# Performance work log

Hardware: AMD Instinct MI355X
Metric: run time of the kernel (lower is better)

## Reference

```python
import jax, jax.numpy as jnp
import numpy as np

N_NODES = 100000


def _graph_conv_right(feat, src, dst, W, b, n_nodes):
    # DGL GraphConv(norm='right'): since in_feats > out_feats, apply weight first,
    # then sum-aggregate messages over edges, divide by in-degree (clamped >= 1),
    # add bias, then relu activation.
    h = feat @ W                                   # [N, out]
    msg = jnp.take(h, src, axis=0)                 # [E, out] gather from source nodes
    agg = jax.ops.segment_sum(msg, dst, num_segments=n_nodes)  # [N, out]
    deg = jax.ops.segment_sum(jnp.ones_like(dst, dtype=feat.dtype), dst,
                              num_segments=n_nodes)
    deg = jnp.clip(deg, 1.0, None)                 # allow_zero_in_degree
    out = agg / deg[:, None] + b
    return jax.nn.relu(out)


def setup_inputs() -> dict:
    key = jax.random.key(0)
    ks = jax.random.split(key, 6)
    n_edges = 3200000
    in_dim, hidden_dim, out_dim = 128, 32, 12
    features = jax.random.normal(ks[0], (N_NODES, in_dim), dtype=jnp.float32)
    src = jax.random.randint(ks[1], (n_edges,), 0, N_NODES, dtype=jnp.int64 if jax.config.jax_enable_x64 else jnp.int32)
    dst = jax.random.randint(ks[2], (n_edges,), 0, N_NODES, dtype=jnp.int64 if jax.config.jax_enable_x64 else jnp.int32)
    W1 = jax.random.normal(ks[3], (in_dim, hidden_dim), dtype=jnp.float32) * (1.0 / np.sqrt(in_dim))
    b1 = jnp.zeros((hidden_dim,), dtype=jnp.float32)
    W2 = jax.random.normal(ks[4], (hidden_dim, out_dim), dtype=jnp.float32) * (1.0 / np.sqrt(hidden_dim))
    b2 = jnp.zeros((out_dim,), dtype=jnp.float32)
    return {"features": features, "src": src, "dst": dst,
            "W1": W1, "b1": b1, "W2": W2, "b2": b2}


def reference(features, src, dst, W1, b1, W2, b2):
    x = _graph_conv_right(features, src, dst, W1, b1, N_NODES)
    x = jax.nn.relu(x)  # extra F.relu after layer1 (idempotent, kept for fidelity)
    x = _graph_conv_right(x, src, dst, W2, b2, N_NODES)
    return x
```

## Files before the change

kernel.cpp:

```cpp
#include <hip/hip_runtime.h>
#include <hip/hip_fp16.h>

#define N_IN   128
#define HID    32
#define ODIM   12
#define RNODES 128
#define NBMAX  800
#define NBK2   1024
#define BCAP   4608
#define CHUNK  4096

__global__ __launch_bounds__(256) void gemm1_kernel(const float* __restrict__ feat,
                                                    const float* __restrict__ W1,
                                                    __half* __restrict__ h1, int nNodes) {
    __shared__ float sF[64 * 132];
    __shared__ float sW[N_IN * HID];
    const int tid = threadIdx.x;
    const int nb  = blockIdx.x * 64;

    {
        const float4* Wv  = (const float4*)W1;
        float4*       sWv = (float4*)sW;
        #pragma unroll
        for (int i = 0; i < 4; ++i) sWv[tid + 256 * i] = Wv[tid + 256 * i];
    }
    #pragma unroll
    for (int i = 0; i < 8; ++i) {
        int f   = tid + 256 * i;
        int row = f >> 5;
        int c4  = f & 31;
        int n   = nb + row;
        float4 v = make_float4(0.f, 0.f, 0.f, 0.f);
        if (n < nNodes) v = *(const float4*)(feat + (size_t)n * N_IN + c4 * 4);
        *(float4*)(sF + row * 132 + c4 * 4) = v;
    }
    __syncthreads();

    const int og = tid & 7;
    const int ng = tid >> 3;
    const int o0 = og * 4;
    const float* f0 = sF + ng * 132;
    const float* f1 = sF + (ng + 32) * 132;

    float acc0[4] = {0.f, 0.f, 0.f, 0.f};
    float acc1[4] = {0.f, 0.f, 0.f, 0.f};
    #pragma unroll 8
    for (int k = 0; k < N_IN; k += 4) {
        float4 a0 = *(const float4*)(f0 + k);
        float4 a1 = *(const float4*)(f1 + k);
        const float a0v[4] = {a0.x, a0.y, a0.z, a0.w};
        const float a1v[4] = {a1.x, a1.y, a1.z, a1.w};
        #pragma unroll
        for (int j = 0; j < 4; ++j) {
            float4 w = *(const float4*)(sW + (k + j) * HID + o0);
            acc0[0] += a0v[j] * w.x; acc0[1] += a0v[j] * w.y;
            acc0[2] += a0v[j] * w.z; acc0[3] += a0v[j] * w.w;
            acc1[0] += a1v[j] * w.x; acc1[1] += a1v[j] * w.y;
            acc1[2] += a1v[j] * w.z; acc1[3] += a1v[j] * w.w;
        }
    }
    int n0 = nb + ng, n1 = nb + ng + 32;
    if (n0 < nNodes) {
        union { __half2 h[2]; float2 f; } u;
        u.h[0] = __floats2half2_rn(acc0[0], acc0[1]);
        u.h[1] = __floats2half2_rn(acc0[2], acc0[3]);
        *(float2*)(h1 + (size_t)n0 * HID + o0) = u.f;
    }
    if (n1 < nNodes) {
        union { __half2 h[2]; float2 f; } u;
        u.h[0] = __floats2half2_rn(acc1[0], acc1[1]);
        u.h[1] = __floats2half2_rn(acc1[2], acc1[3]);
        *(float2*)(h1 + (size_t)n1 * HID + o0) = u.f;
    }
}

__global__ __launch_bounds__(512) void bplace_kernel(const int* __restrict__ src,
                                                     const int* __restrict__ dst,
                                                     int* __restrict__ bcur,
                                                     int* __restrict__ pairs, int nEdges) {
    __shared__ int      lh[NBK2];
    __shared__ int      lcur[NBK2];
    __shared__ int      gofs[NBK2];
    __shared__ int      sAux[512];
    __shared__ int      lst[CHUNK];
    __shared__ unsigned short lbk[CHUNK];

    const int tid  = threadIdx.x;
    const int base = blockIdx.x * CHUNK;
    const int m    = min(CHUNK, nEdges - base);

    lh[tid] = 0; lh[tid + 512] = 0;
    __syncthreads();

    int4 dv[2], sv[2];
    bool ok[2];
    #pragma unroll
    for (int k = 0; k < 2; ++k) {
        int e = base + k * 2048 + tid * 4;
        ok[k] = (e < nEdges);
        if (ok[k]) {
            dv[k] = *(const int4*)(dst + e);
            sv[k] = *(const int4*)(src + e);
        }
    }
    #pragma unroll
    for (int k = 0; k < 2; ++k) {
        if (ok[k]) {
            atomicAdd(&lh[dv[k].x >> 7], 1);
            atomicAdd(&lh[dv[k].y >> 7], 1);
            atomicAdd(&lh[dv[k].z >> 7], 1);
            atomicAdd(&lh[dv[k].w >> 7], 1);
        }
    }
    __syncthreads();

    int c0 = lh[2 * tid], c1 = lh[2 * tid + 1];
    int tsum = c0 + c1;
    sAux[tid] = tsum;
    __syncthreads();
    int inc = tsum;
    for (int off = 1; off < 512; off <<= 1) {
        int t = (tid >= off) ? sAux[tid - off] : 0;
        __syncthreads();
        inc += t;
        sAux[tid] = inc;
        __syncthreads();
    }
    int excl = inc - tsum;
    lh[2 * tid]       = excl;
    lh[2 * tid + 1]   = excl + c0;
    lcur[2 * tid]     = excl;
    lcur[2 * tid + 1] = excl + c0;
    gofs[2 * tid]     = (c0 > 0) ? atomicAdd(&bcur[2 * tid], c0) : 0;
    gofs[2 * tid + 1] = (c1 > 0) ? atomicAdd(&bcur[2 * tid + 1], c1) : 0;
    __syncthreads();

    #pragma unroll
    for (int k = 0; k < 2; ++k) {
        if (ok[k]) {
            int b, p;
            b = dv[k].x >> 7; p = atomicAdd(&lcur[b], 1); lst[p] = ((dv[k].x & 127) << 17) | sv[k].x; lbk[p] = (unsigned short)b;
            b = dv[k].y >> 7; p = atomicAdd(&lcur[b], 1); lst[p] = ((dv[k].y & 127) << 17) | sv[k].y; lbk[p] = (unsigned short)b;
            b = dv[k].z >> 7; p = atomicAdd(&lcur[b], 1); lst[p] = ((dv[k].z & 127) << 17) | sv[k].z; lbk[p] = (unsigned short)b;
            b = dv[k].w >> 7; p = atomicAdd(&lcur[b], 1); lst[p] = ((dv[k].w & 127) << 17) | sv[k].w; lbk[p] = (unsigned short)b;
        }
    }
    __syncthreads();

    for (int i = tid; i < m; i += 512) {
        int b = lbk[i];
        int rank = gofs[b] + (i - lh[b]);
        if (rank < BCAP) pairs[(size_t)b * BCAP + rank] = lst[i];
    }
}

__global__ __launch_bounds__(512) void agg1_kernel(const __half* __restrict__ h1,
                                                   const int* __restrict__ bcur,
                                                   int* __restrict__ pairs,
                                                   const float* __restrict__ b1,
                                                   const float* __restrict__ W2,
                                                   __half* __restrict__ h2,
                                                   float* __restrict__ rdeg,
                                                   int* __restrict__ rowstartg,
                                                   int* __restrict__ countg, int nNodes) {
    __shared__ int   sorted[BCAP];
    __shared__ int   hist[RNODES];
    __shared__ int   scn[RNODES];
    __shared__ int   cur[RNODES];
    __shared__ float sW2[HID * ODIM];
    const int tid = threadIdx.x;
    const int bkt = blockIdx.x;
    const int cnt = min(bcur[bkt], BCAP);
    const size_t pb = (size_t)bkt * BCAP;

    if (tid < RNODES) hist[tid] = 0;
    if (tid < 96) ((float4*)sW2)[tid] = ((const float4*)W2)[tid];
    __syncthreads();

    for (int i = tid; i < cnt; i += 512) atomicAdd(&hist[pairs[pb + i] >> 17], 1);
    __syncthreads();

    int v0 = (tid < RNODES) ? hist[tid] : 0;
    if (tid < RNODES) scn[tid] = v0;
    __syncthreads();
    int inc = v0;
    for (int off = 1; off < RNODES; off <<= 1) {
        int t = (tid < RNODES && tid >= off) ? scn[tid - off] : 0;
        __syncthreads();
        if (tid < RNODES) { inc += t; scn[tid] = inc; }
        __syncthreads();
    }
    if (tid < RNODES) { scn[tid] = inc - v0; cur[tid] = inc - v0; }
    __syncthreads();

    for (int i = tid; i < cnt; i += 512) {
        int v = pairs[pb + i];
        int pos = atomicAdd(&cur[v >> 17], 1);
        sorted[pos] = v & 0x1FFFF;
    }
    __syncthreads();

    for (int i = tid; i < cnt; i += 512) pairs[pb + i] = sorted[i];
    if (tid < RNODES) {
        int n = bkt * RNODES + tid;
        if (n < nNodes) {
            rowstartg[n] = (int)pb + scn[tid];
            countg[n]    = hist[tid];
        }
    }

    const int c   = tid & 15;
    const int grp = tid >> 4;
    const __half2* h1v = (const __half2*)h1;
    const int col = (c < ODIM) ? c : 0;

    #pragma unroll
    for (int g = 0; g < 4; ++g) {
        int nl = g * 32 + grp;
        int n  = bkt * RNODES + nl;
        if (n >= nNodes) continue;
        int dcnt = hist[nl];
        int beg  = scn[nl];
        int end  = beg + dcnt;

        float2 s0 = {0.f, 0.f}, s1 = {0.f, 0.f}, s2 = {0.f, 0.f}, s3 = {0.f, 0.f};
        int i = beg;
        for (; i + 8 <= end; i += 8) {
            int e0 = sorted[i],     e1 = sorted[i + 1], e2 = sorted[i + 2], e3 = sorted[i + 3];
            int e4 = sorted[i + 4], e5 = sorted[i + 5], e6 = sorted[i + 6], e7 = sorted[i + 7];
            float2 f0 = __half22float2(h1v[(size_t)e0 * 16 + c]);
            float2 f1 = __half22float2(h1v[(size_t)e1 * 16 + c]);
            float2 f2 = __half22float2(h1v[(size_t)e2 * 16 + c]);
            float2 f3 = __half22float2(h1v[(size_t)e3 * 16 + c]);
            float2 f4 = __half22float2(h1v[(size_t)e4 * 16 + c]);
            float2 f5 = __half22float2(h1v[(size_t)e5 * 16 + c]);
            float2 f6 = __half22float2(h1v[(size_t)e6 * 16 + c]);
            float2 f7 = __half22float2(h1v[(size_t)e7 * 16 + c]);
            s0.x += f0.x; s0.y += f0.y;  s1.x += f1.x; s1.y += f1.y;
            s2.x += f2.x; s2.y += f2.y;  s3.x += f3.x; s3.y += f3.y;
            s0.x += f4.x; s0.y += f4.y;  s1.x += f5.x; s1.y += f5.y;
            s2.x += f6.x; s2.y += f6.y;  s3.x += f7.x; s3.y += f7.y;
        }
        for (; i + 4 <= end; i += 4) {
            int e0 = sorted[i], e1 = sorted[i + 1], e2 = sorted[i + 2], e3 = sorted[i + 3];
            float2 f0 = __half22float2(h1v[(size_t)e0 * 16 + c]);
            float2 f1 = __half22float2(h1v[(size_t)e1 * 16 + c]);
            float2 f2 = __half22float2(h1v[(size_t)e2 * 16 + c]);
            float2 f3 = __half22float2(h1v[(size_t)e3 * 16 + c]);
            s0.x += f0.x; s0.y += f0.y;  s1.x += f1.x; s1.y += f1.y;
            s2.x += f2.x; s2.y += f2.y;  s3.x += f3.x; s3.y += f3.y;
        }
        for (; i < end; ++i) {
            float2 f = __half22float2(h1v[(size_t)sorted[i] * 16 + c]);
            s0.x += f.x; s0.y += f.y;
        }
        float sumx = (s0.x + s1.x) + (s2.x + s3.x);
        float sumy = (s0.y + s1.y) + (s2.y + s3.y);

        float rd = 1.f / (float)(dcnt < 1 ? 1 : dcnt);
        float x0 = sumx * rd + b1[2 * c];
        float x1 = sumy * rd + b1[2 * c + 1];
        x0 = x0 > 0.f ? x0 : 0.f;
        x1 = x1 > 0.f ? x1 : 0.f;

        float acc = 0.f;
        #pragma unroll
        for (int k = 0; k < 16; ++k) {
            float xk0 = __shfl(x0, k, 16);
            float xk1 = __shfl(x1, k, 16);
            acc += xk0 * sW2[(2 * k) * ODIM + col] + xk1 * sW2[(2 * k + 1) * ODIM + col];
        }
        if (c < ODIM) h2[(size_t)n * ODIM + c] = __float2half(acc);
        if (c == 0)   rdeg[n] = rd;
    }
}

__global__ __launch_bounds__(256) void agg2_kernel(const __half* __restrict__ h2,
                                                   const int* __restrict__ rowstartg,
                                                   const int* __restrict__ countg,
                                                   const int* __restrict__ eidx,
                                                   const float* __restrict__ rdeg,
                                                   const float* __restrict__ b2,
                                                   float* __restrict__ out, int nNodes) {
    const int tid = threadIdx.x;
    const int n = blockIdx.x * 32 + (tid >> 3);
    const int c = tid & 7;
    if (n >= nNodes) return;

    const int cnt = countg[n];
    const int beg = rowstartg[n];
    const int end = beg + cnt;
    const int cc  = (c < 6) ? c : 0;
    const __half2* h2v = (const __half2*)h2;

    float2 s0 = {0.f, 0.f}, s1 = {0.f, 0.f}, s2 = {0.f, 0.f}, s3 = {0.f, 0.f};
    int i = beg;
    for (; i + 8 <= end; i += 8) {
        int e0 = eidx[i],     e1 = eidx[i + 1], e2 = eidx[i + 2], e3 = eidx[i + 3];
        int e4 = eidx[i + 4], e5 = eidx[i + 5], e6 = eidx[i + 6], e7 = eidx[i + 7];
        float2 f0 = __half22float2(h2v[(size_t)e0 * 6 + cc]);
        float2 f1 = __half22float2(h2v[(size_t)e1 * 6 + cc]);
        float2 f2 = __half22float2(h2v[(size_t)e2 * 6 + cc]);
        float2 f3 = __half22float2(h2v[(size_t)e3 * 6 + cc]);
        float2 f4 = __half22float2(h2v[(size_t)e4 * 6 + cc]);
        float2 f5 = __half22float2(h2v[(size_t)e5 * 6 + cc]);
        float2 f6 = __half22float2(h2v[(size_t)e6 * 6 + cc]);
        float2 f7 = __half22float2(h2v[(size_t)e7 * 6 + cc]);
        s0.x += f0.x; s0.y += f0.y;  s1.x += f1.x; s1.y += f1.y;
        s2.x += f2.x; s2.y += f2.y;  s3.x += f3.x; s3.y += f3.y;
        s0.x += f4.x; s0.y += f4.y;  s1.x += f5.x; s1.y += f5.y;
        s2.x += f6.x; s2.y += f6.y;  s3.x += f7.x; s3.y += f7.y;
    }
    for (; i + 4 <= end; i += 4) {
        int e0 = eidx[i], e1 = eidx[i + 1], e2 = eidx[i + 2], e3 = eidx[i + 3];
        float2 f0 = __half22float2(h2v[(size_t)e0 * 6 + cc]);
        float2 f1 = __half22float2(h2v[(size_t)e1 * 6 + cc]);
        float2 f2 = __half22float2(h2v[(size_t)e2 * 6 + cc]);
        float2 f3 = __half22float2(h2v[(size_t)e3 * 6 + cc]);
        s0.x += f0.x; s0.y += f0.y;  s1.x += f1.x; s1.y += f1.y;
        s2.x += f2.x; s2.y += f2.y;  s3.x += f3.x; s3.y += f3.y;
    }
    for (; i < end; ++i) {
        float2 f = __half22float2(h2v[(size_t)eidx[i] * 6 + cc]);
        s0.x += f.x; s0.y += f.y;
    }
    float sumx = (s0.x + s1.x) + (s2.x + s3.x);
    float sumy = (s0.y + s1.y) + (s2.y + s3.y);

    float rd = rdeg[n];
    float w0 = sumx * rd + b2[2 * cc];
    float w1 = sumy * rd + b2[2 * cc + 1];
    w0 = w0 > 0.f ? w0 : 0.f;
    w1 = w1 > 0.f ? w1 : 0.f;
    if (c < 6) *(float2*)(out + (size_t)n * ODIM + 2 * c) = make_float2(w0, w1);
}

extern "C" void kernel_launch(void* const* d_in, const int* in_sizes, int n_in,
                              void* d_out, int out_size, void* d_ws, size_t ws_size,
                              hipStream_t stream) {
    const float* feat = (const float*)d_in[0];
    const int*   src  = (const int*)d_in[1];
    const int*   dst  = (const int*)d_in[2];
    const float* W1   = (const float*)d_in[3];
    const float* b1   = (const float*)d_in[4];
    const float* W2   = (const float*)d_in[5];
    const float* b2   = (const float*)d_in[6];
    float* out = (float*)d_out;

    const int nEdges = in_sizes[1];
    const int nNodes = in_sizes[0] / N_IN;
    const int nb     = (nNodes + RNODES - 1) / RNODES;

    __half* h1       = (__half*)d_ws;
    __half* h2       = h1 + (size_t)nNodes * HID;
    float*  rdeg     = (float*)(h2 + (size_t)nNodes * ODIM);
    int*    rowstart = (int*)(rdeg + nNodes);
    int*    countg   = rowstart + nNodes;
    int*    bcur     = countg + nNodes;
    int*    pairs    = bcur + NBK2;

    hipMemsetAsync(bcur, 0, NBK2 * sizeof(int), stream);

    gemm1_kernel<<<(nNodes + 63) / 64, 256, 0, stream>>>(feat, W1, h1, nNodes);
    bplace_kernel<<<(nEdges + CHUNK - 1) / CHUNK, 512, 0, stream>>>(src, dst, bcur, pairs, nEdges);
    agg1_kernel<<<nb, 512, 0, stream>>>(h1, bcur, pairs, b1, W2, h2, rdeg, rowstart, countg, nNodes);
    agg2_kernel<<<(nNodes + 31) / 32, 256, 0, stream>>>(h2, rowstart, countg, pairs, rdeg, b2, out, nNodes);
}
```

Baseline: 235.5 us.

## Split CSR sort from layer-1 aggregation and double bucket-placement chunk size

The fused per-bucket sort+aggregate kernel is split in two. A csr_kernel sorts the edges inside each bucket and writes the CSR row starts and counts. A separate fine-grained agg1_kernel then gathers over global edge indices with 16 nodes per 256-thread block, which gives far more blocks than the roughly 782 bucket blocks of the fused version. The bplace chunk is also doubled to 8192 edges per block, so there are fewer global atomic offset reservations. In exchange, the sorted indices are re-read from global memory instead of LDS, there is an extra launch, and bplace uses more registers and LDS per block.

```diff
diff --git a/kernel.cpp b/kernel.cpp
--- a/kernel.cpp
+++ b/kernel.cpp
@@ -8,7 +8,7 @@
 #define NBMAX  800
 #define NBK2   1024
 #define BCAP   4608
-#define CHUNK  4096
+#define CHUNK  8192
 
 __global__ __launch_bounds__(256) void gemm1_kernel(const float* __restrict__ feat,
                                                     const float* __restrict__ W1,
@@ -92,10 +92,10 @@
     lh[tid] = 0; lh[tid + 512] = 0;
     __syncthreads();
 
-    int4 dv[2], sv[2];
-    bool ok[2];
-    #pragma unroll
-    for (int k = 0; k < 2; ++k) {
+    int4 dv[4], sv[4];
+    bool ok[4];
+    #pragma unroll
+    for (int k = 0; k < 4; ++k) {
         int e = base + k * 2048 + tid * 4;
         ok[k] = (e < nEdges);
         if (ok[k]) {
@@ -104,7 +104,7 @@
         }
     }
     #pragma unroll
-    for (int k = 0; k < 2; ++k) {
+    for (int k = 0; k < 4; ++k) {
         if (ok[k]) {
             atomicAdd(&lh[dv[k].x >> 7], 1);
             atomicAdd(&lh[dv[k].y >> 7], 1);
@@ -136,7 +136,7 @@
     __syncthreads();
 
     #pragma unroll
-    for (int k = 0; k < 2; ++k) {
+    for (int k = 0; k < 4; ++k) {
         if (ok[k]) {
             int b, p;
             b = dv[k].x >> 7; p = atomicAdd(&lcur[b], 1); lst[p] = ((dv[k].x & 127) << 17) | sv[k].x; lbk[p] = (unsigned short)b;
@@ -154,27 +154,20 @@
     }
 }
 
-__global__ __launch_bounds__(512) void agg1_kernel(const __half* __restrict__ h1,
-                                                   const int* __restrict__ bcur,
-                                                   int* __restrict__ pairs,
-                                                   const float* __restrict__ b1,
-                                                   const float* __restrict__ W2,
-                                                   __half* __restrict__ h2,
-                                                   float* __restrict__ rdeg,
-                                                   int* __restrict__ rowstartg,
-                                                   int* __restrict__ countg, int nNodes) {
-    __shared__ int   sorted[BCAP];
-    __shared__ int   hist[RNODES];
-    __shared__ int   scn[RNODES];
-    __shared__ int   cur[RNODES];
-    __shared__ float sW2[HID * ODIM];
+__global__ __launch_bounds__(512) void csr_kernel(const int* __restrict__ bcur,
+                                                  int* __restrict__ pairs,
+                                                  int* __restrict__ rowstartg,
+                                                  int* __restrict__ countg, int nNodes) {
+    __shared__ int sorted[BCAP];
+    __shared__ int hist[RNODES];
+    __shared__ int scn[RNODES];
+    __shared__ int cur[RNODES];
     const int tid = threadIdx.x;
     const int bkt = blockIdx.x;
     const int cnt = min(bcur[bkt], BCAP);
     const size_t pb = (size_t)bkt * BCAP;
 
     if (tid < RNODES) hist[tid] = 0;
-    if (tid < 96) ((float4*)sW2)[tid] = ((const float4*)W2)[tid];
     __syncthreads();
 
     for (int i = tid; i < cnt; i += 512) atomicAdd(&hist[pairs[pb + i] >> 17], 1);
@@ -190,7 +183,16 @@
         if (tid < RNODES) { inc += t; scn[tid] = inc; }
         __syncthreads();
     }
-    if (tid < RNODES) { scn[tid] = inc - v0; cur[tid] = inc - v0; }
+    if (tid < RNODES) {
+        int excl = inc - v0;
+        scn[tid] = excl;
+        cur[tid] = excl;
+        int n = bkt * RNODES + tid;
+        if (n < nNodes) {
+            rowstartg[n] = (int)pb + excl;
+            countg[n]    = v0;
+        }
+    }
     __syncthreads();
 
     for (int i = tid; i < cnt; i += 512) {
@@ -201,78 +203,80 @@
     __syncthreads();
 
     for (int i = tid; i < cnt; i += 512) pairs[pb + i] = sorted[i];
-    if (tid < RNODES) {
-        int n = bkt * RNODES + tid;
-        if (n < nNodes) {
-            rowstartg[n] = (int)pb + scn[tid];
-            countg[n]    = hist[tid];
-        }
-    }
-
-    const int c   = tid & 15;
-    const int grp = tid >> 4;
+}
+
+__global__ __launch_bounds__(256) void agg1_kernel(const __half* __restrict__ h1,
+                                                   const int* __restrict__ rowstartg,
+                                                   const int* __restrict__ countg,
+                                                   const int* __restrict__ eidx,
+                                                   const float* __restrict__ b1,
+                                                   const float* __restrict__ W2,
+                                                   __half* __restrict__ h2,
+                                                   float* __restrict__ rdeg, int nNodes) {
+    __shared__ float sW2[HID * ODIM];
+    const int tid = threadIdx.x;
+    if (tid < 96) ((float4*)sW2)[tid] = ((const float4*)W2)[tid];
+    __syncthreads();
+
+    const int n = blockIdx.x * 16 + (tid >> 4);
+    const int c = tid & 15;
+    if (n >= nNodes) return;
+
+    const int cnt = countg[n];
+    const int beg = rowstartg[n];
+    const int end = beg + cnt;
     const __half2* h1v = (const __half2*)h1;
     const int col = (c < ODIM) ? c : 0;
 
-    #pragma unroll
-    for (int g = 0; g < 4; ++g) {
-        int nl = g * 32 + grp;
-        int n  = bkt * RNODES + nl;
-        if (n >= nNodes) continue;
-        int dcnt = hist[nl];
-        int beg  = scn[nl];
-        int end  = beg + dcnt;
-
-        float2 s0 = {0.f, 0.f}, s1 = {0.f, 0.f}, s2 = {0.f, 0.f}, s3 = {0.f, 0.f};
-        int i = beg;
-        for (; i + 8 <= end; i += 8) {
-            int e0 = sorted[i],     e1 = sorted[i + 1], e2 = sorted[i + 2], e3 = sorted[i + 3];
-            int e4 = sorted[i + 4], e5 = sorted[i + 5], e6 = sorted[i + 6], e7 = sorted[i + 7];
-            float2 f0 = __half22float2(h1v[(size_t)e0 * 16 + c]);
-            float2 f1 = __half22float2(h1v[(size_t)e1 * 16 + c]);
-            float2 f2 = __half22float2(h1v[(size_t)e2 * 16 + c]);
-            float2 f3 = __half22float2(h1v[(size_t)e3 * 16 + c]);
-            float2 f4 = __half22float2(h1v[(size_t)e4 * 16 + c]);
-            float2 f5 = __half22float2(h1v[(size_t)e5 * 16 + c]);
-            float2 f6 = __half22float2(h1v[(size_t)e6 * 16 + c]);
-            float2 f7 = __half22float2(h1v[(size_t)e7 * 16 + c]);
-            s0.x += f0.x; s0.y += f0.y;  s1.x += f1.x; s1.y += f1.y;
-            s2.x += f2.x; s2.y += f2.y;  s3.x += f3.x; s3.y += f3.y;
-            s0.x += f4.x; s0.y += f4.y;  s1.x += f5.x; s1.y += f5.y;
-            s2.x += f6.x; s2.y += f6.y;  s3.x += f7.x; s3.y += f7.y;
-        }
-        for (; i + 4 <= end; i += 4) {
-            int e0 = sorted[i], e1 = sorted[i + 1], e2 = sorted[i + 2], e3 = sorted[i + 3];
-            float2 f0 = __half22float2(h1v[(size_t)e0 * 16 + c]);
-            float2 f1 = __half22float2(h1v[(size_t)e1 * 16 + c]);
-            float2 f2 = __half22float2(h1v[(size_t)e2 * 16 + c]);
-            float2 f3 = __half22float2(h1v[(size_t)e3 * 16 + c]);
-            s0.x += f0.x; s0.y += f0.y;  s1.x += f1.x; s1.y += f1.y;
-            s2.x += f2.x; s2.y += f2.y;  s3.x += f3.x; s3.y += f3.y;
-        }
-        for (; i < end; ++i) {
-            float2 f = __half22float2(h1v[(size_t)sorted[i] * 16 + c]);
-            s0.x += f.x; s0.y += f.y;
-        }
-        float sumx = (s0.x + s1.x) + (s2.x + s3.x);
-        float sumy = (s0.y + s1.y) + (s2.y + s3.y);
-
-        float rd = 1.f / (float)(dcnt < 1 ? 1 : dcnt);
-        float x0 = sumx * rd + b1[2 * c];
-        float x1 = sumy * rd + b1[2 * c + 1];
-        x0 = x0 > 0.f ? x0 : 0.f;
-        x1 = x1 > 0.f ? x1 : 0.f;
-
-        float acc = 0.f;
-        #pragma unroll
-        for (int k = 0; k < 16; ++k) {
-            float xk0 = __shfl(x0, k, 16);
-            float xk1 = __shfl(x1, k, 16);
-            acc += xk0 * sW2[(2 * k) * ODIM + col] + xk1 * sW2[(2 * k + 1) * ODIM + col];
-        }
-        if (c < ODIM) h2[(size_t)n * ODIM + c] = __float2half(acc);
-        if (c == 0)   rdeg[n] = rd;
-    }
+    float2 s0 = {0.f, 0.f}, s1 = {0.f, 0.f}, s2 = {0.f, 0.f}, s3 = {0.f, 0.f};
+    int i = beg;
+    for (; i + 8 <= end; i += 8) {
+        int e0 = eidx[i],     e1 = eidx[i + 1], e2 = eidx[i + 2], e3 = eidx[i + 3];
+        int e4 = eidx[i + 4], e5 = eidx[i + 5], e6 = eidx[i + 6], e7 = eidx[i + 7];
+        float2 f0 = __half22float2(h1v[(size_t)e0 * 16 + c]);
+        float2 f1 = __half22float2(h1v[(size_t)e1 * 16 + c]);
+        float2 f2 = __half22float2(h1v[(size_t)e2 * 16 + c]);
+        float2 f3 = __half22float2(h1v[(size_t)e3 * 16 + c]);
+        float2 f4 = __half22float2(h1v[(size_t)e4 * 16 + c]);
+        float2 f5 = __half22float2(h1v[(size_t)e5 * 16 + c]);
+        float2 f6 = __half22float2(h1v[(size_t)e6 * 16 + c]);
+        float2 f7 = __half22float2(h1v[(size_t)e7 * 16 + c]);
+        s0.x += f0.x; s0.y += f0.y;  s1.x += f1.x; s1.y += f1.y;
+        s2.x += f2.x; s2.y += f2.y;  s3.x += f3.x; s3.y += f3.y;
+        s0.x += f4.x; s0.y += f4.y;  s1.x += f5.x; s1.y += f5.y;
+        s2.x += f6.x; s2.y += f6.y;  s3.x += f7.x; s3.y += f7.y;
+    }
+    for (; i + 4 <= end; i += 4) {
+        int e0 = eidx[i], e1 = eidx[i + 1], e2 = eidx[i + 2], e3 = eidx[i + 3];
+        float2 f0 = __half22float2(h1v[(size_t)e0 * 16 + c]);
+        float2 f1 = __half22float2(h1v[(size_t)e1 * 16 + c]);
+        float2 f2 = __half22float2(h1v[(size_t)e2 * 16 + c]);
+        float2 f3 = __half22float2(h1v[(size_t)e3 * 16 + c]);
+        s0.x += f0.x; s0.y += f0.y;  s1.x += f1.x; s1.y += f1.y;
+        s2.x += f2.x; s2.y += f2.y;  s3.x += f3.x; s3.y += f3.y;
+    }
+    for (; i < end; ++i) {
+        float2 f = __half22float2(h1v[(size_t)eidx[i] * 16 + c]);
+        s0.x += f.x; s0.y += f.y;
+    }
+    float sumx = (s0.x + s1.x) + (s2.x + s3.x);
+    float sumy = (s0.y + s1.y) + (s2.y + s3.y);
+
+    float rd = 1.f / (float)(cnt < 1 ? 1 : cnt);
+    float x0 = sumx * rd + b1[2 * c];
+    float x1 = sumy * rd + b1[2 * c + 1];
+    x0 = x0 > 0.f ? x0 : 0.f;
+    x1 = x1 > 0.f ? x1 : 0.f;
+
+    float acc = 0.f;
+    #pragma unroll
+    for (int k = 0; k < 16; ++k) {
+        float xk0 = __shfl(x0, k, 16);
+        float xk1 = __shfl(x1, k, 16);
+        acc += xk0 * sW2[(2 * k) * ODIM + col] + xk1 * sW2[(2 * k + 1) * ODIM + col];
+    }
+    if (c < ODIM) h2[(size_t)n * ODIM + c] = __float2half(acc);
+    if (c == 0)   rdeg[n] = rd;
 }
 
 __global__ __launch_bounds__(256) void agg2_kernel(const __half* __restrict__ h2,
@@ -363,6 +367,7 @@
 
     gemm1_kernel<<<(nNodes + 63) / 64, 256, 0, stream>>>(feat, W1, h1, nNodes);
     bplace_kernel<<<(nEdges + CHUNK - 1) / CHUNK, 512, 0, stream>>>(src, dst, bcur, pairs, nEdges);
-    agg1_kernel<<<nb, 512, 0, stream>>>(h1, bcur, pairs, b1, W2, h2, rdeg, rowstart, countg, nNodes);
+    csr_kernel<<<nb, 512, 0, stream>>>(bcur, pairs, rowstart, countg, nNodes);
+    agg1_kernel<<<(nNodes + 15) / 16, 256, 0, stream>>>(h1, rowstart, countg, pairs, b1, W2, h2, rdeg, nNodes);
     agg2_kernel<<<(nNodes + 31) / 32, 256, 0, stream>>>(h2, rowstart, countg, pairs, rdeg, b2, out, nNodes);
 }
```

Result: faster. 228.1 us (-3.1%).
